# Optimization experiments

Hardware: AMD Instinct MI355X
Metric: run time of the kernel (lower is better)

Reference implementation:

```python
import jax, jax.numpy as jnp
import numpy as np

GAMMA = 1.0        # softmin temperature (module default)
BANDWIDTH = 1024.0 # Sakoe-Chiba band half-width (module default float(1024))
WARP = 0.0         # extra penalty on non-diagonal (insert/delete) moves
BIG = 1e10         # finite stand-in for +inf (safe under logsumexp/vjp)
B, N, M, DF = 32, 512, 512, 64


def _softdtw(X, Y, X_len, Y_len):
    """Soft-DTW via anti-diagonal wavefront scan.

    R[i, j] = D[i-1, j-1] + softmin_gamma(R[i-1,j-1], R[i-1,j]+warp, R[i,j-1]+warp)
    with R[0,0]=0, borders = +inf; loss[b] = R[X_len[b], Y_len[b]].
    Cells on anti-diagonal d = i+j depend only on diagonals d-1 and d-2,
    so we scan over d carrying the last two diagonals, each stored as a
    vector over i in [0, N] (vectorized over batch and diagonal cells).
    """
    Bb, Nn, _ = X.shape
    Mm = Y.shape[1]
    # Squared-Euclidean cost matrix [B, N, M]
    D = (jnp.sum(X * X, -1)[:, :, None]
         + jnp.sum(Y * Y, -1)[:, None, :]
         - 2.0 * jnp.einsum('bnd,bmd->bnm', X, Y))

    ii = jnp.arange(Nn + 1)                               # row index along diagonal
    r2 = jnp.full((Bb, Nn + 1), BIG, jnp.float32).at[:, 0].set(0.0)  # diag d=0: R[0,0]=0
    r1 = jnp.full((Bb, Nn + 1), BIG, jnp.float32)                    # diag d=1: all inf

    def step(carry, dd):
        r2, r1 = carry
        jj = dd - ii                                      # column index j = d - i
        valid = (ii >= 1) & (jj >= 1) & (jj <= Mm) & (jnp.abs(ii - jj) <= BANDWIDTH)
        Dd = D[:, jnp.clip(ii - 1, 0, Nn - 1), jnp.clip(jj - 1, 0, Mm - 1)]  # [B, N+1]
        big_col = jnp.full((Bb, 1), BIG, jnp.float32)
        r2_im1 = jnp.concatenate([big_col, r2[:, :-1]], 1)  # R[i-1, j-1]
        r1_im1 = jnp.concatenate([big_col, r1[:, :-1]], 1)  # R[i-1, j]
        z = jnp.stack([r2_im1, r1_im1 + WARP, r1 + WARP], 0)
        soft = -GAMMA * jax.nn.logsumexp(-z / GAMMA, axis=0)  # softmin
        cur = jnp.where(valid[None, :], Dd + soft, BIG)
        return (r1, cur), cur

    _, diags = jax.lax.scan(step, (r2, r1), jnp.arange(2, Nn + Mm + 1))
    # diags[k] holds anti-diagonal d = k + 2, so R[i, j] = diags[i + j - 2][:, i]
    b = jnp.arange(Bb)
    return diags[X_len + Y_len - 2, b, X_len]


def setup_inputs() -> dict:
    key = jax.random.key(0)
    k1, k2, k3, k4 = jax.random.split(key, 4)
    X = jax.random.normal(k1, (B, N, DF), jnp.float32)
    Y = jax.random.normal(k2, (B, M, DF), jnp.float32)
    X_len = jax.random.randint(k3, (B,), 3 * N // 4, N + 1).astype(jnp.int32)
    Y_len = jax.random.randint(k4, (B,), 3 * M // 4, M + 1).astype(jnp.int32)
    return {"X": X, "Y": Y, "X_len": X_len, "Y_len": Y_len}


def reference(X, Y, X_len, Y_len):
    return _softdtw(X, Y, X_len, Y_len)
```

## Files before the change

### kernel.cpp

```cpp
#include <hip/hip_runtime.h>
#include <hip/hip_fp16.h>
#include <cstddef>

#define Bc   32
#define Nc   512
#define Mc   512
#define DFc  64
#define BIGC 1.0e10f
#define LOG2E_F 1.4426950408889634f
#define LN2_F   0.6931471805599453f
#define SQRT_LOG2E_F 1.2011224087864498f

typedef unsigned int uint32;
typedef _Float16 f16x8 __attribute__((ext_vector_type(8)));
typedef float    f32x4 __attribute__((ext_vector_type(4)));

__device__ __forceinline__ float dpp_shr1(float oldv, float src) {
    return __int_as_float(__builtin_amdgcn_update_dpp(
        __float_as_int(oldv), __float_as_int(src), 0x138, 0xf, 0xf, false));
}
__device__ __forceinline__ float dpp_shr1_nc(float src) {
    return __int_as_float(__builtin_amdgcn_mov_dpp(
        __float_as_int(src), 0x138, 0xf, 0xf, false));
}
__device__ __forceinline__ float rl(float v, int lane) {
    return __int_as_float(__builtin_amdgcn_readlane(__float_as_int(v), lane));
}

__device__ __forceinline__ float softmin3m(float a, float b, float c) {
    float mn = fminf(fminf(a, b), c);
    float mx = fmaxf(fmaxf(a, b), c);
    float md = __builtin_amdgcn_fmed3f(a, b, c);
    uint32 b1 = (uint32)fmaf(mn - mx, 8388608.0f, 1065353216.0f);
    uint32 b2 = (uint32)fmaf(mn - md, 8388608.0f, 1065353216.0f);
    float E = 1.0f + (__int_as_float(b1) + __int_as_float(b2));
    return fmaf((float)__float_as_uint(E), -1.1920929e-7f, mn);
}

__global__ __launch_bounds__(256) void dist_kernel(
    const float* __restrict__ X, const float* __restrict__ Y,
    uint32* __restrict__ Dsk)
{
    __shared__ __align__(16) unsigned char SMEM[35840];
    unsigned short* XsH = (unsigned short*)SMEM;
    unsigned short* YsH = (unsigned short*)(SMEM + 16384);
    uint32* P  = (uint32*)SMEM;
    float* xx2 = (float*)(SMEM + 34816);
    float* yy2 = (float*)(SMEM + 35328);

    const int b     = blockIdx.z;
    const int strip = blockIdx.y;
    const int J     = blockIdx.x;
    const int tid   = threadIdx.x;

    const float* Xg = X + ((size_t)b * Nc + strip * 128) * DFc;
    const float* Yg = Y + ((size_t)b * Mc + J * 128) * DFc;

#pragma unroll
    for (int it = 0; it < 8; ++it) {
        int e4 = it * 256 + tid;
        int n = e4 >> 4, k4 = (e4 & 15) * 4;
        float4 v = ((const float4*)Xg)[e4];
        float sx = v.x * SQRT_LOG2E_F, sy = v.y * SQRT_LOG2E_F;
        float sz = v.z * SQRT_LOG2E_F, sw = v.w * SQRT_LOG2E_F;
        __half2 h01 = __floats2half2_rn(sx, sy);
        __half2 h23 = __floats2half2_rn(sz, sw);
        int ho = (k4 + 8 * (n & 7)) & 63;
        uint2 u; u.x = *(uint32*)&h01; u.y = *(uint32*)&h23;
        *(uint2*)&XsH[n * 64 + ho] = u;
        float p = sx * sx + sy * sy + sz * sz + sw * sw;
        p += __shfl_xor(p, 1);
        p += __shfl_xor(p, 2);
        p += __shfl_xor(p, 4);
        p += __shfl_xor(p, 8);
        if ((tid & 15) == 0) xx2[n] = p + 127.0f;
    }
#pragma unroll
    for (int it = 0; it < 8; ++it) {
        int e4 = it * 256 + tid;
        int m = e4 >> 4, k4 = (e4 & 15) * 4;
        float4 v = ((const float4*)Yg)[e4];
        float sx = v.x * SQRT_LOG2E_F, sy = v.y * SQRT_LOG2E_F;
        float sz = v.z * SQRT_LOG2E_F, sw = v.w * SQRT_LOG2E_F;
        __half2 h01 = __floats2half2_rn(sx, sy);
        __half2 h23 = __floats2half2_rn(sz, sw);
        int ho = (k4 + 8 * (m & 7)) & 63;
        uint2 u; u.x = *(uint32*)&h01; u.y = *(uint32*)&h23;
        *(uint2*)&YsH[m * 64 + ho] = u;
        float p = sx * sx + sy * sy + sz * sz + sw * sw;
        p += __shfl_xor(p, 1);
        p += __shfl_xor(p, 2);
        p += __shfl_xor(p, 4);
        p += __shfl_xor(p, 8);
        if ((tid & 15) == 0) yy2[m] = p;
    }
    __syncthreads();

    const int l  = tid & 63;
    const int w  = tid >> 6;
    const int lr = l & 15;
    const int lk = l >> 4;

    f32x4 acc[2][8];
#pragma unroll
    for (int rt = 0; rt < 2; ++rt)
#pragma unroll
        for (int ct = 0; ct < 8; ++ct) {
            f32x4 z = {0.f, 0.f, 0.f, 0.f};
            acc[rt][ct] = z;
        }

#pragma unroll
    for (int ks = 0; ks < 2; ++ks) {
        f16x8 af[2], bf[8];
#pragma unroll
        for (int rt = 0; rt < 2; ++rt) {
            int row = w * 32 + rt * 16 + lr;
            int ho = (ks * 32 + lk * 8 + 8 * (row & 7)) & 63;
            af[rt] = *(const f16x8*)&XsH[row * 64 + ho];
        }
#pragma unroll
        for (int ct = 0; ct < 8; ++ct) {
            int col = ct * 16 + lr;
            int ho = (ks * 32 + lk * 8 + 8 * (col & 7)) & 63;
            bf[ct] = *(const f16x8*)&YsH[col * 64 + ho];
        }
#pragma unroll
        for (int rt = 0; rt < 2; ++rt)
#pragma unroll
            for (int ct = 0; ct < 8; ++ct)
                acc[rt][ct] = __builtin_amdgcn_mfma_f32_16x16x32_f16(
                    af[rt], bf[ct], acc[rt][ct], 0, 0, 0);
    }
    __syncthreads();

#pragma unroll
    for (int rt = 0; rt < 2; ++rt) {
        int rbase = w * 32 + rt * 16 + 4 * lk;
        f32x4 xr = *(const f32x4*)&xx2[rbase];
        int p0 = rbase >> 1;
#pragma unroll
        for (int ct = 0; ct < 8; ++ct) {
            int c = ct * 16 + lr;
            float yv = yy2[c];
            f32x4 a = acc[rt][ct];
            float d0 = xr[0] + yv - 2.0f * a[0];
            float d1 = xr[1] + yv - 2.0f * a[1];
            float d2 = xr[2] + yv - 2.0f * a[2];
            float d3 = xr[3] + yv - 2.0f * a[3];
            __half2 h0 = __floats2half2_rn(d0, d1);
            __half2 h1 = __floats2half2_rn(d2, d3);
            P[c * 67 + p0]     = *(uint32*)&h0;
            P[c * 67 + p0 + 1] = *(uint32*)&h1;
        }
    }
    __syncthreads();

    const int q = tid >> 6;
    uint4* outt = (uint4*)Dsk + (((size_t)b * 4 + strip) * 4 + J) * 4096;
    const uint32* Pl = P + l;
#pragma unroll
    for (int gi = 0; gi < 16; ++gi) {
        int g = q + 4 * gi;
        int ka = 4 * g - 2 * l;
        int c0 = min(max(ka,     0), 127);
        int c1 = min(max(ka + 1, 0), 127);
        int c2 = min(max(ka + 2, 0), 127);
        int c3 = min(max(ka + 3, 0), 127);
        uint32 p0 = Pl[c0 * 67];
        uint32 p1 = Pl[c1 * 67];
        uint32 p2 = Pl[c2 * 67];
        uint32 p3 = Pl[c3 * 67];
        uint4 v;
        v.x = (p0 & 0xffffu) | (p1 << 16);
        v.y = (p0 >> 16)     | (p1 & 0xffff0000u);
        v.z = (p2 & 0xffffu) | (p3 << 16);
        v.w = (p2 >> 16)     | (p3 & 0xffff0000u);
        outt[g * 64 + l] = v;
    }
}

#define SSTEP(T, dAw, dBw, PH1)                                            \
  {                                                                        \
    float2 fA = __half22float2(*(const __half2*)&(dAw));                   \
    float2 fB = __half22float2(*(const __half2*)&(dBw));                   \
    float u1, u2;                                                          \
    if (PH1) {                                                             \
      u1 = dpp_shr1(rl(Fodd, (T) - 1), pub1);                              \
      u2 = dpp_shr1(rl(Fev,  (T) - 1), curB);                              \
    } else {                                                               \
      u1 = dpp_shr1_nc(pub1);                                              \
      u2 = dpp_shr1_nc(curB);                                              \
    }                                                                      \
    float A1 = softmin3m(diagA, u1, curA) + fA.x;                          \
    float A2 = softmin3m(u1, u2, A1) + fA.y;                               \
    float B1 = softmin3m(curA, A1, curB) + fB.x;                           \
    float B2 = softmin3m(A1, A2, B1) + fB.y;                               \
    if ((T) == scap)                                                       \
      capv = useB ? (useC2 ? B2 : B1) : (useC2 ? A2 : A1);                 \
    bool act = (PH1) ? (l < (T)) : (l >= (T) - 64);                        \
    pub1  = act ? B1 : curB;                 \
    curA  = act ? A2 : curA;                                               \
    curB  = act ? B2 : curB;                                               \
    diagA = u2;                                                            \
    if (!(PH1)) { wbase[2 * (T) - 127] = B1; wbase[2 * (T) - 126] = B2; }  \
  }

__global__ __launch_bounds__(256) void scan_kernel(
    const uint32* __restrict__ Dsk,
    const int* __restrict__ X_len, const int* __restrict__ Y_len,
    float* __restrict__ out)
{
    __shared__ __align__(16) float Frow[4][520];
    __shared__ float dumpArr[136];

    const int tid = threadIdx.x;
    const int l  = tid & 63;
    const int wl = __builtin_amdgcn_readfirstlane(tid >> 6);
    const int bb = blockIdx.x;

    const int xl = X_len[bb], yl = Y_len[bb];
    const int wxl  = (xl - 1) >> 7;
    const int iw   = (xl - 1) & 127;
    const int lcap = iw >> 1;
    const int useB = iw & 1;
    const int Jcap = (yl - 1) >> 7;
    const int ycol = yl - (Jcap << 7);
    const int useC2 = 1 - (ycol & 1);
    const int tcap = ((ycol + 1) >> 1) + lcap;
    const int kmax = wxl + Jcap;

    const bool is63 = (l == 63);

    if (l == 0) Frow[wl][0] = BIGC;
    __syncthreads();

    float curA = BIGC, curB = BIGC, pub1 = BIGC;
    float diagA = BIGC;
    float capv = 0.0f;

    for (int k = 0; k <= kmax; ++k) {
        int J = k - wl;
        if (wl <= wxl && 0 <= J && J <= Jcap) {
            const int j0 = J << 7;
            float Fodd, Fev, f0;
            if (wl > 0) {
                Fodd = Frow[wl - 1][j0 + 1 + 2 * l];
                Fev  = Frow[wl - 1][j0 + 2 + 2 * l];
                f0   = Frow[wl - 1][j0];
            } else {
                Fodd = BIGC; Fev = BIGC;
                f0 = (J == 0) ? 0.0f : BIGC;
            }
            diagA = (l == 0) ? f0 : diagA;

            const char* tb = (const char*)Dsk +
                (((((size_t)bb * 4 + wl) * 4) + J) * 4096) * 16;
            const int voff = l * 16;
            const int scap = (wl == wxl && J == Jcap) ? tcap : -1000;
            float* wbase = is63 ? (&Frow[wl][j0]) : (dumpArr + 4);

            uint4 dreg[4];
            dreg[0] = *(const uint4*)(tb + voff);
            dreg[1] = *(const uint4*)(tb + voff + 1024);
            dreg[2] = *(const uint4*)(tb + voff + 2048);
            dreg[3] = *(const uint4*)(tb + voff + 3072);

#pragma unroll 1
            for (int m = 0; m < 8; ++m) {
#pragma unroll
                for (int q = 0; q < 4; ++q) {
                    const int g = m * 4 + q;
                    uint4 dc = dreg[q];
                    dreg[q] = *(const uint4*)(tb + voff + (g + 4) * 1024);
                    SSTEP(2 * g + 1, dc.x, dc.y, true)
                    SSTEP(2 * g + 2, dc.z, dc.w, true)
                }
            }
            wbase[1] = pub1;
            wbase[2] = curB;

#pragma unroll 1
            for (int m = 8; m < 15; ++m) {
#pragma unroll
                for (int q = 0; q < 4; ++q) {
                    const int g = m * 4 + q;
                    uint4 dc = dreg[q];
                    dreg[q] = *(const uint4*)(tb + voff + (g + 4) * 1024);
                    SSTEP(2 * g + 1, dc.x, dc.y, false)
                    SSTEP(2 * g + 2, dc.z, dc.w, false)
                }
            }
#pragma unroll
            for (int q = 0; q < 4; ++q) {
                const int g = 60 + q;
                uint4 dc = dreg[q];
                SSTEP(2 * g + 1, dc.x, dc.y, false)
                if (g < 63) { SSTEP(2 * g + 2, dc.z, dc.w, false) }
            }
        }
        __syncthreads();
    }

    if (wl == wxl) {
        float o = rl(capv, lcap);
        if (l == 0) out[bb] = o * LN2_F;
    }
}

extern "C" void kernel_launch(void* const* d_in, const int* in_sizes, int n_in,
                              void* d_out, int out_size, void* d_ws, size_t ws_size,
                              hipStream_t stream)
{
    const float* X  = (const float*)d_in[0];
    const float* Y  = (const float*)d_in[1];
    const int*   xl = (const int*)d_in[2];
    const int*   yl = (const int*)d_in[3];
    float* out = (float*)d_out;
    uint32* Dsk = (uint32*)d_ws;

    dist_kernel<<<dim3(4, 4, Bc), 256, 0, stream>>>(X, Y, Dsk);
    scan_kernel<<<Bc, 256, 0, stream>>>(Dsk, xl, yl, out);
}
```

Measured before the change: 201.2 us.

## Rewrite soft-DTW scan as single-wave 8-row-per-lane skewed wavefront

The scan kernel moves from four waves, each owning a 128-row strip and handing boundaries through shared memory with block-wide barriers, to a single 64-lane wave. Each lane owns 8 consecutive rows and advances two columns per step, passing boundary values to the next lane through DPP shifts. The distance kernel now writes the cost tile in a skewed layout indexed by (column+row, row), so every lane reads its 8x2 cell block with two 16-byte loads per step. This removes the inter-wave barriers and the shared-memory boundary traffic, but the serial chain per lane becomes longer and each block launches only one wave.

```diff
diff --git a/kernel.cpp b/kernel.cpp
--- a/kernel.cpp
+++ b/kernel.cpp
@@ -11,6 +11,8 @@
 #define LN2_F   0.6931471805599453f
 #define SQRT_LOG2E_F 1.2011224087864498f
 
+#define BSTRIDE 653312
+
 typedef unsigned int uint32;
 typedef _Float16 f16x8 __attribute__((ext_vector_type(8)));
 typedef float    f32x4 __attribute__((ext_vector_type(4)));
@@ -18,10 +20,6 @@
 __device__ __forceinline__ float dpp_shr1(float oldv, float src) {
     return __int_as_float(__builtin_amdgcn_update_dpp(
         __float_as_int(oldv), __float_as_int(src), 0x138, 0xf, 0xf, false));
-}
-__device__ __forceinline__ float dpp_shr1_nc(float src) {
-    return __int_as_float(__builtin_amdgcn_mov_dpp(
-        __float_as_int(src), 0x138, 0xf, 0xf, false));
 }
 __device__ __forceinline__ float rl(float v, int lane) {
     return __int_as_float(__builtin_amdgcn_readlane(__float_as_int(v), lane));
@@ -44,7 +42,7 @@
     __shared__ __align__(16) unsigned char SMEM[35840];
     unsigned short* XsH = (unsigned short*)SMEM;
     unsigned short* YsH = (unsigned short*)(SMEM + 16384);
-    uint32* P  = (uint32*)SMEM;
+    unsigned short* P2 = (unsigned short*)SMEM;
     float* xx2 = (float*)(SMEM + 34816);
     float* yy2 = (float*)(SMEM + 35328);
 
@@ -138,7 +136,6 @@
     for (int rt = 0; rt < 2; ++rt) {
         int rbase = w * 32 + rt * 16 + 4 * lk;
         f32x4 xr = *(const f32x4*)&xx2[rbase];
-        int p0 = rbase >> 1;
 #pragma unroll
         for (int ct = 0; ct < 8; ++ct) {
             int c = ct * 16 + lr;
@@ -150,162 +147,114 @@
             float d3 = xr[3] + yv - 2.0f * a[3];
             __half2 h0 = __floats2half2_rn(d0, d1);
             __half2 h1 = __floats2half2_rn(d2, d3);
-            P[c * 67 + p0]     = *(uint32*)&h0;
-            P[c * 67 + p0 + 1] = *(uint32*)&h1;
+            uint2 u; u.x = *(uint32*)&h0; u.y = *(uint32*)&h1;
+            *(uint2*)&P2[c * 136 + rbase] = u;
         }
     }
     __syncthreads();
 
-    const int q = tid >> 6;
-    uint4* outt = (uint4*)Dsk + (((size_t)b * 4 + strip) * 4 + J) * 4096;
-    const uint32* Pl = P + l;
-#pragma unroll
-    for (int gi = 0; gi < 16; ++gi) {
-        int g = q + 4 * gi;
-        int ka = 4 * g - 2 * l;
-        int c0 = min(max(ka,     0), 127);
-        int c1 = min(max(ka + 1, 0), 127);
-        int c2 = min(max(ka + 2, 0), 127);
-        int c3 = min(max(ka + 3, 0), 127);
-        uint32 p0 = Pl[c0 * 67];
-        uint32 p1 = Pl[c1 * 67];
-        uint32 p2 = Pl[c2 * 67];
-        uint32 p3 = Pl[c3 * 67];
-        uint4 v;
-        v.x = (p0 & 0xffffu) | (p1 << 16);
-        v.y = (p0 >> 16)     | (p1 & 0xffff0000u);
-        v.z = (p2 & 0xffffu) | (p3 << 16);
-        v.w = (p2 >> 16)     | (p3 & 0xffff0000u);
-        outt[g * 64 + l] = v;
-    }
-}
-
-#define SSTEP(T, dAw, dBw, PH1)                                            \
+    char* ob = (char*)Dsk + (size_t)b * BSTRIDE;
+#pragma unroll
+    for (int k = 0; k < 4; ++k) {
+        int slot = k * 256 + tid;
+        int a  = slot >> 6;
+        int cl = slot & 63;
+        int ii = 16 * strip + a;
+        int cc = 64 * J + cl;
+        uint4 r0 = *(const uint4*)&P2[(2 * cl) * 136 + 8 * a];
+        uint4 r1 = *(const uint4*)&P2[(2 * cl + 1) * 136 + 8 * a];
+        uint4 w0, w1;
+        w0.x = (r0.x & 0xffffu) | (r1.x << 16);
+        w0.y = (r0.x >> 16)     | (r1.x & 0xffff0000u);
+        w0.z = (r0.y & 0xffffu) | (r1.y << 16);
+        w0.w = (r0.y >> 16)     | (r1.y & 0xffff0000u);
+        w1.x = (r0.z & 0xffffu) | (r1.z << 16);
+        w1.y = (r0.z >> 16)     | (r1.z & 0xffff0000u);
+        w1.z = (r0.w & 0xffffu) | (r1.w << 16);
+        w1.w = (r0.w >> 16)     | (r1.w & 0xffff0000u);
+        char* dst = ob + ((size_t)(cc + ii) * 64 + ii) * 32;
+        *(uint4*)dst = w0;
+        *(uint4*)(dst + 16) = w1;
+    }
+}
+
+#define STEP8(JJ)                                                          \
   {                                                                        \
-    float2 fA = __half22float2(*(const __half2*)&(dAw));                   \
-    float2 fB = __half22float2(*(const __half2*)&(dBw));                   \
-    float u1, u2;                                                          \
-    if (PH1) {                                                             \
-      u1 = dpp_shr1(rl(Fodd, (T) - 1), pub1);                              \
-      u2 = dpp_shr1(rl(Fev,  (T) - 1), curB);                              \
-    } else {                                                               \
-      u1 = dpp_shr1_nc(pub1);                                              \
-      u2 = dpp_shr1_nc(curB);                                              \
+    float u1 = dpp_shr1(bigc, O7p);                                        \
+    float u2 = dpp_shr1(bigc, E7p);                                        \
+    float upO = u1, upE = u2;                                              \
+    uint4 da = dregA[JJ], db = dregB[JJ];                                  \
+    {                                                                      \
+      int cc = s0 + ((JJ) + 4) - i;                                        \
+      cc = min(max(cc, 0), 255);                                           \
+      int vo = ((cc + i) << 11) + (i << 5);                                \
+      dregA[JJ] = *(const uint4*)(tbase + vo);                             \
+      dregB[JJ] = *(const uint4*)(tbase + vo + 16);                        \
     }                                                                      \
-    float A1 = softmin3m(diagA, u1, curA) + fA.x;                          \
-    float A2 = softmin3m(u1, u2, A1) + fA.y;                               \
-    float B1 = softmin3m(curA, A1, curB) + fB.x;                           \
-    float B2 = softmin3m(A1, A2, B1) + fB.y;                               \
-    if ((T) == scap)                                                       \
-      capv = useB ? (useC2 ? B2 : B1) : (useC2 ? A2 : A1);                 \
-    bool act = (PH1) ? (l < (T)) : (l >= (T) - 64);                        \
-    pub1  = act ? B1 : curB;                 \
-    curA  = act ? A2 : curA;                                               \
-    curB  = act ? B2 : curB;                                               \
-    diagA = u2;                                                            \
-    if (!(PH1)) { wbase[2 * (T) - 127] = B1; wbase[2 * (T) - 126] = B2; }  \
+    const uint32 dw[8] = {da.x, da.y, da.z, da.w, db.x, db.y, db.z, db.w}; \
+    _Pragma("unroll")                                                      \
+    for (int r = 0; r < 8; ++r) {                                          \
+      float2 f = __half22float2(*(const __half2*)&dw[r]);                  \
+      float O = softmin3m(diag[r], upO, curE[r]) + f.x;                    \
+      float E = softmin3m(upO, upE, O) + f.y;                              \
+      diag[r] = upE;                                                       \
+      curE[r] = E;                                                         \
+      Ov[r] = O; Ev[r] = E;                                                \
+      upO = O; upE = E;                                                    \
+    }                                                                      \
+    O7p = Ov[7]; E7p = Ev[7];                                              \
+    if (s0 + (JJ) == scap) {                                               \
+      float vv = useE ? Ev[0] : Ov[0];                                     \
+      _Pragma("unroll")                                                    \
+      for (int r = 1; r < 8; ++r)                                          \
+        vv = (rcap == r) ? (useE ? Ev[r] : Ov[r]) : vv;                    \
+      capv = (i == icap) ? vv : capv;                                      \
+    }                                                                      \
   }
 
-__global__ __launch_bounds__(256) void scan_kernel(
+__global__ __launch_bounds__(64) void scan_kernel(
     const uint32* __restrict__ Dsk,
     const int* __restrict__ X_len, const int* __restrict__ Y_len,
     float* __restrict__ out)
 {
-    __shared__ __align__(16) float Frow[4][520];
-    __shared__ float dumpArr[136];
-
-    const int tid = threadIdx.x;
-    const int l  = tid & 63;
-    const int wl = __builtin_amdgcn_readfirstlane(tid >> 6);
+    const int i  = threadIdx.x;
     const int bb = blockIdx.x;
 
     const int xl = X_len[bb], yl = Y_len[bb];
-    const int wxl  = (xl - 1) >> 7;
-    const int iw   = (xl - 1) & 127;
-    const int lcap = iw >> 1;
-    const int useB = iw & 1;
-    const int Jcap = (yl - 1) >> 7;
-    const int ycol = yl - (Jcap << 7);
-    const int useC2 = 1 - (ycol & 1);
-    const int tcap = ((ycol + 1) >> 1) + lcap;
-    const int kmax = wxl + Jcap;
-
-    const bool is63 = (l == 63);
-
-    if (l == 0) Frow[wl][0] = BIGC;
-    __syncthreads();
-
-    float curA = BIGC, curB = BIGC, pub1 = BIGC;
-    float diagA = BIGC;
-    float capv = 0.0f;
-
-    for (int k = 0; k <= kmax; ++k) {
-        int J = k - wl;
-        if (wl <= wxl && 0 <= J && J <= Jcap) {
-            const int j0 = J << 7;
-            float Fodd, Fev, f0;
-            if (wl > 0) {
-                Fodd = Frow[wl - 1][j0 + 1 + 2 * l];
-                Fev  = Frow[wl - 1][j0 + 2 + 2 * l];
-                f0   = Frow[wl - 1][j0];
-            } else {
-                Fodd = BIGC; Fev = BIGC;
-                f0 = (J == 0) ? 0.0f : BIGC;
-            }
-            diagA = (l == 0) ? f0 : diagA;
-
-            const char* tb = (const char*)Dsk +
-                (((((size_t)bb * 4 + wl) * 4) + J) * 4096) * 16;
-            const int voff = l * 16;
-            const int scap = (wl == wxl && J == Jcap) ? tcap : -1000;
-            float* wbase = is63 ? (&Frow[wl][j0]) : (dumpArr + 4);
-
-            uint4 dreg[4];
-            dreg[0] = *(const uint4*)(tb + voff);
-            dreg[1] = *(const uint4*)(tb + voff + 1024);
-            dreg[2] = *(const uint4*)(tb + voff + 2048);
-            dreg[3] = *(const uint4*)(tb + voff + 3072);
+    const int icap = (xl - 1) >> 3;
+    const int rcap = (xl - 1) & 7;
+    const int ccap = (yl - 1) >> 1;
+    const int useE = (yl - 1) & 1;
+    const int scap = ccap + icap;
+
+    const char* tbase = (const char*)Dsk + (size_t)bb * BSTRIDE;
+
+    const float bigc = BIGC;
+    float curE[8], diag[8], Ov[8], Ev[8];
+#pragma unroll
+    for (int r = 0; r < 8; ++r) { curE[r] = BIGC; diag[r] = BIGC; }
+    diag[0] = (i == 0) ? 0.0f : BIGC;
+    float O7p = BIGC, E7p = BIGC, capv = 0.0f;
+
+    uint4 dregA[4], dregB[4];
+#pragma unroll
+    for (int j = 0; j < 4; ++j) {
+        int cc = min(max(j - i, 0), 255);
+        int vo = ((cc + i) << 11) + (i << 5);
+        dregA[j] = *(const uint4*)(tbase + vo);
+        dregB[j] = *(const uint4*)(tbase + vo + 16);
+    }
 
 #pragma unroll 1
-            for (int m = 0; m < 8; ++m) {
-#pragma unroll
-                for (int q = 0; q < 4; ++q) {
-                    const int g = m * 4 + q;
-                    uint4 dc = dreg[q];
-                    dreg[q] = *(const uint4*)(tb + voff + (g + 4) * 1024);
-                    SSTEP(2 * g + 1, dc.x, dc.y, true)
-                    SSTEP(2 * g + 2, dc.z, dc.w, true)
-                }
-            }
-            wbase[1] = pub1;
-            wbase[2] = curB;
-
-#pragma unroll 1
-            for (int m = 8; m < 15; ++m) {
-#pragma unroll
-                for (int q = 0; q < 4; ++q) {
-                    const int g = m * 4 + q;
-                    uint4 dc = dreg[q];
-                    dreg[q] = *(const uint4*)(tb + voff + (g + 4) * 1024);
-                    SSTEP(2 * g + 1, dc.x, dc.y, false)
-                    SSTEP(2 * g + 2, dc.z, dc.w, false)
-                }
-            }
-#pragma unroll
-            for (int q = 0; q < 4; ++q) {
-                const int g = 60 + q;
-                uint4 dc = dreg[q];
-                SSTEP(2 * g + 1, dc.x, dc.y, false)
-                if (g < 63) { SSTEP(2 * g + 2, dc.z, dc.w, false) }
-            }
-        }
-        __syncthreads();
-    }
-
-    if (wl == wxl) {
-        float o = rl(capv, lcap);
-        if (l == 0) out[bb] = o * LN2_F;
-    }
+    for (int s0 = 0; s0 <= scap; s0 += 4) {
+        STEP8(0)
+        STEP8(1)
+        STEP8(2)
+        STEP8(3)
+    }
+
+    float o = rl(capv, icap);
+    if (i == 0) out[bb] = o * LN2_F;
 }
 
 extern "C" void kernel_launch(void* const* d_in, const int* in_sizes, int n_in,
@@ -320,5 +269,5 @@
     uint32* Dsk = (uint32*)d_ws;
 
     dist_kernel<<<dim3(4, 4, Bc), 256, 0, stream>>>(X, Y, Dsk);
-    scan_kernel<<<Bc, 256, 0, stream>>>(Dsk, xl, yl, out);
-}
+    scan_kernel<<<Bc, 64, 0, stream>>>(Dsk, xl, yl, out);
+}
```

After: 222.8 us. 1.11x slower.
